# Optimization experiments

Measured on AMD Instinct MI355X. Metric: run time of the kernel, lower is better.

Reference implementation:

```python
import jax, jax.numpy as jnp
import numpy as np

N_NODES = 100000
N_EDGES = 1600000
IN_FEATS = 64
HIDDEN = 128


def setup_inputs() -> dict:
    key = jax.random.key(0)
    k1, k2, k3, k4 = jax.random.split(key, 4)
    X = jax.random.normal(k1, (N_NODES, IN_FEATS), dtype=jnp.float32)
    edge_index = jax.random.randint(k2, (2, N_EDGES), 0, N_NODES, dtype=jnp.int64)
    W1 = jax.random.normal(k3, (IN_FEATS, HIDDEN), dtype=jnp.float32) * (1.0 / np.sqrt(IN_FEATS))
    b1 = jnp.zeros((HIDDEN,), dtype=jnp.float32)
    W2 = jax.random.normal(k4, (HIDDEN, 1), dtype=jnp.float32) * (1.0 / np.sqrt(HIDDEN))
    b2 = jnp.zeros((1,), dtype=jnp.float32)
    return {"X": X, "edge_index": edge_index, "W1": W1, "b1": b1, "W2": W2, "b2": b2}


def _gcn_conv(X, src, dst, norm, W, b, n_nodes):
    # GCNConv: out = D^{-1/2} (A + I) D^{-1/2} (X @ W) + b
    h = X @ W                       # [N, out_feats]
    msg = h[src] * norm[:, None]    # gather + per-edge scale
    out = jax.ops.segment_sum(msg, dst, num_segments=n_nodes)
    return out + b


def _norm_and_loops(edge_index, n_nodes):
    # add self loops and compute symmetric normalization coefficients
    loop = jnp.arange(n_nodes, dtype=edge_index.dtype)
    src = jnp.concatenate([edge_index[0], loop])
    dst = jnp.concatenate([edge_index[1], loop])
    deg = jax.ops.segment_sum(jnp.ones_like(dst, dtype=jnp.float32), dst,
                              num_segments=n_nodes)  # deg >= 1 (self loop)
    dinv = jax.lax.rsqrt(deg)
    norm = dinv[src] * dinv[dst]    # [E + N]
    return src, dst, norm


def reference(X, edge_index, W1, b1, W2, b2):
    n_nodes = X.shape[0]
    src, dst, norm = _norm_and_loops(edge_index, n_nodes)
    h = jax.nn.relu(_gcn_conv(X, src, dst, norm, W1, b1, n_nodes))
    # dropout omitted (stochastic; identity for deterministic reference)
    out = _gcn_conv(h, src, dst, norm, W2, b2, n_nodes)
    return out
```

## Files before the change

kernel.cpp:

```cpp
#include <hip/hip_runtime.h>
#include <hip/hip_fp16.h>


#define NNODES 100000
#define INF 64
#define HID 128
#define MAXBK 128
#define TILE_E 16384

using half8 = __attribute__((ext_vector_type(8))) _Float16;
using f32x4 = __attribute__((ext_vector_type(4))) float;

__global__ __launch_bounds__(1024) void k_thist(const int* __restrict__ dstA,
                                                int* __restrict__ tileCnt, int nE) {
    __shared__ int h[MAXBK];
    int tid = threadIdx.x;
    if (tid < MAXBK) h[tid] = 0;
    __syncthreads();
    int base = blockIdx.x * TILE_E;
#pragma unroll
    for (int k = 0; k < 16; ++k) {
        int e = base + k * 1024 + tid;
        if (e < nE) atomicAdd(&h[((unsigned)dstA[e]) >> 10], 1);
    }
    __syncthreads();
    if (tid < MAXBK) tileCnt[blockIdx.x * MAXBK + tid] = h[tid];
}

__global__ __launch_bounds__(1024) void k_bscan(const int* __restrict__ tileCnt,
                                                int* __restrict__ tileBase,
                                                int* __restrict__ bBase,
                                                int* __restrict__ rowPtr,
                                                int n, int nbk, int nt) {
    __shared__ int part[8][MAXBK];
    __shared__ int colScan[MAXBK];
    int b = threadIdx.x & (MAXBK - 1);
    int tg = threadIdx.x >> 7;
    int cpg = (nt + 7) / 8;
    int tlo = tg * cpg, thi = min(tlo + cpg, nt);
    int sum = 0;
    for (int t = tlo; t < thi; ++t) sum += tileCnt[t * MAXBK + b];
    part[tg][b] = sum;
    __syncthreads();
    int coff = 0;
    for (int g = 0; g < tg; ++g) coff += part[g][b];
    int ctot = 0;
#pragma unroll
    for (int g = 0; g < 8; ++g) ctot += part[g][b];
    if (tg == 0) colScan[b] = ctot;
    __syncthreads();
    for (int off = 1; off < MAXBK; off <<= 1) {
        int u = (tg == 0 && b >= off) ? colScan[b - off] : 0;
        __syncthreads();
        if (tg == 0) colScan[b] += u;
        __syncthreads();
    }
    int colBase = colScan[b] - ctot;
    if (tg == 0 && b < nbk) bBase[b] = colBase;
    if (tg == 0 && b == nbk - 1) { bBase[nbk] = colScan[b]; rowPtr[n] = colScan[b]; }
    int run = colBase + coff;
    for (int t = tlo; t < thi; ++t) {
        tileBase[t * MAXBK + b] = run;
        run += tileCnt[t * MAXBK + b];
    }
}

__global__ __launch_bounds__(1024) void k_bin(const int* __restrict__ srcA,
                                              const int* __restrict__ dstA,
                                              const int* __restrict__ tileBase,
                                              unsigned* __restrict__ binned, int nE) {
    __shared__ int myb[MAXBK];
    __shared__ int cur[MAXBK];
    int tid = threadIdx.x;
    if (tid < MAXBK) {
        myb[tid] = tileBase[blockIdx.x * MAXBK + tid];
        cur[tid] = 0;
    }
    __syncthreads();
    int base = blockIdx.x * TILE_E;
#pragma unroll
    for (int k = 0; k < 16; ++k) {
        int e = base + k * 1024 + tid;
        if (e < nE) {
            int d = dstA[e];
            int s = srcA[e];
            int bk = ((unsigned)d) >> 10;
            int off = atomicAdd(&cur[bk], 1);
            binned[myb[bk] + off] = ((unsigned)(d & 1023) << 17) | (unsigned)s;
        }
    }
}

__global__ __launch_bounds__(1024) void k_csr(const unsigned* __restrict__ binned,
                                              const int* __restrict__ bBase,
                                              int* __restrict__ rowPtr,
                                              float* __restrict__ dinv,
                                              int* __restrict__ eSrc, int n) {
    __shared__ int hist[1024];
    __shared__ int curs[1024];
    int tid = threadIdx.x;
    int b = blockIdx.x;
    int lo = bBase[b], hi = bBase[b + 1];
    hist[tid] = 0;
    __syncthreads();
    for (int i = lo + tid; i < hi; i += 1024)
        atomicAdd(&hist[binned[i] >> 17], 1);
    __syncthreads();
    int own = hist[tid];
    for (int off = 1; off < 1024; off <<= 1) {
        int u = (tid >= off) ? hist[tid - off] : 0;
        __syncthreads();
        hist[tid] += u;
        __syncthreads();
    }
    int pos0 = lo + hist[tid] - own;
    curs[tid] = pos0;
    int node = (b << 10) + tid;
    if (node < n) {
        rowPtr[node] = pos0;
        dinv[node] = rsqrtf((float)(own + 1));
    }
    __syncthreads();
    for (int i = lo + tid; i < hi; i += 1024) {
        unsigned v = binned[i];
        int pos = atomicAdd(&curs[v >> 17], 1);
        eSrc[pos] = (int)(v & 0x1FFFFu);
    }
}

__global__ void k_prescale(const float4* __restrict__ X4, const float* __restrict__ dinv,
                           uint4* __restrict__ Xs4, const float* __restrict__ W1,
                           _Float16* __restrict__ W1t, int n) {
    int t = blockIdx.x * blockDim.x + threadIdx.x;
    if (t < n * 8) {
        int node = t >> 3;
        int r = t & 7;
        float dD = dinv[node];
        float4 a = X4[(size_t)node * 16 + r * 2];
        float4 b = X4[(size_t)node * 16 + r * 2 + 1];
        __half2 h0 = __float22half2_rn(make_float2(dD * a.x, dD * a.y));
        __half2 h1 = __float22half2_rn(make_float2(dD * a.z, dD * a.w));
        __half2 h2 = __float22half2_rn(make_float2(dD * b.x, dD * b.y));
        __half2 h3 = __float22half2_rn(make_float2(dD * b.z, dD * b.w));
        uint4 o;
        o.x = *(unsigned*)&h0; o.y = *(unsigned*)&h1;
        o.z = *(unsigned*)&h2; o.w = *(unsigned*)&h3;
        Xs4[t] = o;
    } else {
        int i = t - n * 8;
        if (i < HID * INF) {
            int nCol = i >> 6;
            int k = i & 63;
            W1t[i] = (_Float16)W1[k * HID + nCol];
        }
    }
}

__device__ inline void acc8_add(const uint4& v, float* acc) {
    const __half2* hp = (const __half2*)&v;
#pragma unroll
    for (int i = 0; i < 4; ++i) {
        float2 f = __half22float2(hp[i]);
        acc[2 * i]     += f.x;
        acc[2 * i + 1] += f.y;
    }
}

__global__ __launch_bounds__(256) void k_agg_mlp(const uint4* __restrict__ Xs4,
                                                 const int* __restrict__ rowPtr,
                                                 const int* __restrict__ eSrc,
                                                 const float* __restrict__ dinv,
                                                 const uint4* __restrict__ W1t4,
                                                 const float* __restrict__ b1,
                                                 const float* __restrict__ W2,
                                                 float* __restrict__ svs, int n) {
    __shared__ __align__(16) unsigned short W1s[HID * INF];
    __shared__ __align__(16) unsigned short aggS[32 * INF];
    __shared__ float b1s[HID];
    __shared__ float W2s[HID];
    int tid = threadIdx.x;

    for (int i = tid; i < HID * 8; i += 256) {
        int c = i >> 3, cb = i & 7;
        uint4 v = W1t4[i];
        int off = c * 128 + ((cb * 16) ^ ((c & 7) << 4));
        *(uint4*)((char*)W1s + off) = v;
    }
    if (tid < HID) {
        b1s[tid] = b1[tid];
        W2s[tid] = W2[tid];
    }

    int node0 = blockIdx.x * 32;
    int w = tid >> 3;
    int r = tid & 7;
    int node = node0 + w;
    if (node < n) {
        int beg = rowPtr[node];
        int end = rowPtr[node + 1];
        float dD = dinv[node];
        float acc[8];
        {
            uint4 v = Xs4[(size_t)node * 8 + r];
            const __half2* hp = (const __half2*)&v;
#pragma unroll
            for (int i = 0; i < 4; ++i) {
                float2 f = __half22float2(hp[i]);
                acc[2 * i] = f.x;
                acc[2 * i + 1] = f.y;
            }
        }
        int j = beg;
        int aEnd = min(end, (beg + 3) & ~3);
        for (; j < aEnd; ++j) {
            uint4 v = Xs4[(size_t)eSrc[j] * 8 + r];
            acc8_add(v, acc);
        }
        for (; j + 3 < end; j += 4) {
            int4 s4 = *(const int4*)(eSrc + j);
            uint4 v0 = Xs4[(size_t)s4.x * 8 + r];
            uint4 v1 = Xs4[(size_t)s4.y * 8 + r];
            uint4 v2 = Xs4[(size_t)s4.z * 8 + r];
            uint4 v3 = Xs4[(size_t)s4.w * 8 + r];
            acc8_add(v0, acc); acc8_add(v1, acc); acc8_add(v2, acc); acc8_add(v3, acc);
        }
        for (; j < end; ++j) {
            uint4 v = Xs4[(size_t)eSrc[j] * 8 + r];
            acc8_add(v, acc);
        }
        __half2 h0 = __float22half2_rn(make_float2(dD * acc[0], dD * acc[1]));
        __half2 h1 = __float22half2_rn(make_float2(dD * acc[2], dD * acc[3]));
        __half2 h2 = __float22half2_rn(make_float2(dD * acc[4], dD * acc[5]));
        __half2 h3 = __float22half2_rn(make_float2(dD * acc[6], dD * acc[7]));
        uint4 o;
        o.x = *(unsigned*)&h0; o.y = *(unsigned*)&h1;
        o.z = *(unsigned*)&h2; o.w = *(unsigned*)&h3;
        int off = w * 128 + ((r * 16) ^ ((w & 7) << 4));
        *(uint4*)((char*)aggS + off) = o;
    }
    __syncthreads();

    int wave = tid >> 6;
    if (wave < 2) {
        int l = tid & 63;
        int row16 = l & 15;
        int kg = l >> 4;
        int lrow = wave * 16 + row16;
        int swzA = (lrow & 7) << 4;
        half8 a0 = *(const half8*)((const char*)aggS + lrow * 128 + ((kg * 16) ^ swzA));
        half8 a1 = *(const half8*)((const char*)aggS + lrow * 128 + ((64 + kg * 16) ^ swzA));
        float p0 = 0.0f, p1 = 0.0f, p2 = 0.0f, p3 = 0.0f;
#pragma unroll
        for (int nt = 0; nt < 8; ++nt) {
            int c = nt * 16 + row16;
            int swzB = (c & 7) << 4;
            half8 bf0 = *(const half8*)((const char*)W1s + c * 128 + ((kg * 16) ^ swzB));
            half8 bf1 = *(const half8*)((const char*)W1s + c * 128 + ((64 + kg * 16) ^ swzB));
            f32x4 acc4 = {0.0f, 0.0f, 0.0f, 0.0f};
            acc4 = __builtin_amdgcn_mfma_f32_16x16x32_f16(a0, bf0, acc4, 0, 0, 0);
            acc4 = __builtin_amdgcn_mfma_f32_16x16x32_f16(a1, bf1, acc4, 0, 0, 0);
            float b1v = b1s[c];
            float w2v = W2s[c];
            float h;
            h = fmaxf(acc4[0] + b1v, 0.0f); p0 = fmaf(h, w2v, p0);
            h = fmaxf(acc4[1] + b1v, 0.0f); p1 = fmaf(h, w2v, p1);
            h = fmaxf(acc4[2] + b1v, 0.0f); p2 = fmaf(h, w2v, p2);
            h = fmaxf(acc4[3] + b1v, 0.0f); p3 = fmaf(h, w2v, p3);
        }
#pragma unroll
        for (int off = 1; off < 16; off <<= 1) {
            p0 += __shfl_xor(p0, off, 64);
            p1 += __shfl_xor(p1, off, 64);
            p2 += __shfl_xor(p2, off, 64);
            p3 += __shfl_xor(p3, off, 64);
        }
        if (row16 == 0) {
            int nd = node0 + wave * 16 + kg * 4;
            if (nd + 0 < n) svs[nd + 0] = dinv[nd + 0] * p0;
            if (nd + 1 < n) svs[nd + 1] = dinv[nd + 1] * p1;
            if (nd + 2 < n) svs[nd + 2] = dinv[nd + 2] * p2;
            if (nd + 3 < n) svs[nd + 3] = dinv[nd + 3] * p3;
        }
    }
}

__global__ __launch_bounds__(256) void k_out(const int* __restrict__ rowPtr,
                                             const int* __restrict__ eSrc,
                                             const float* __restrict__ dinv,
                                             const float* __restrict__ svs,
                                             const float* __restrict__ b2,
                                             float* __restrict__ out, int n) {
    int t = blockIdx.x * blockDim.x + threadIdx.x;
    int node = t >> 4;
    int r = t & 15;
    if (node >= n) return;
    int beg = rowPtr[node];
    int end = rowPtr[node + 1];
    float p = 0.0f;
    for (int j = beg + r; j < end; j += 16) p += svs[eSrc[j]];
    p += __shfl_xor(p, 1, 16);
    p += __shfl_xor(p, 2, 16);
    p += __shfl_xor(p, 4, 16);
    p += __shfl_xor(p, 8, 16);
    if (r == 0) {
        float dD = dinv[node];
        out[node] = fmaf(dD, p + svs[node], b2[0]);
    }
}

extern "C" void kernel_launch(void* const* d_in, const int* in_sizes, int n_in,
                              void* d_out, int out_size, void* d_ws, size_t ws_size,
                              hipStream_t stream) {
    const float* X  = (const float*)d_in[0];
    const int*   ei = (const int*)d_in[1];
    const float* W1 = (const float*)d_in[2];
    const float* b1 = (const float*)d_in[3];
    const float* W2 = (const float*)d_in[4];
    const float* b2 = (const float*)d_in[5];

    int N = in_sizes[0] / INF;
    int E = in_sizes[1] / 2;
    const int* srcA = ei;
    const int* dstA = ei + E;

    int nt  = (E + TILE_E - 1) / TILE_E;
    int nbk = (N + 1023) >> 10;

    uint4*    Xs4      = (uint4*)d_ws;
    unsigned* binned   = (unsigned*)(Xs4 + (size_t)N * 8);
    int*      eSrc     = (int*)(binned + E);
    _Float16* W1t      = (_Float16*)(eSrc + E);
    int*      tileCnt  = (int*)(W1t + HID * INF);
    int*      tileBase = tileCnt + nt * MAXBK;
    int*      bBase    = tileBase + nt * MAXBK;
    int*      rowPtr   = bBase + nbk + 1;
    float*    dinv     = (float*)(rowPtr + N + 1);
    float*    svs      = dinv + N;
    float*    out      = (float*)d_out;

    k_thist<<<nt, 1024, 0, stream>>>(dstA, tileCnt, E);
    k_bscan<<<1, 1024, 0, stream>>>(tileCnt, tileBase, bBase, rowPtr, N, nbk, nt);
    k_bin<<<nt, 1024, 0, stream>>>(srcA, dstA, tileBase, binned, E);
    k_csr<<<nbk, 1024, 0, stream>>>(binned, bBase, rowPtr, dinv, eSrc, N);
    k_prescale<<<(N * 8 + HID * INF + 255) / 256, 256, 0, stream>>>(
        (const float4*)X, dinv, Xs4, W1, W1t, N);
    k_agg_mlp<<<(N + 31) / 32, 256, 0, stream>>>(Xs4, rowPtr, eSrc, dinv,
                                                 (const uint4*)W1t, b1, W2, svs, N);
    k_out<<<(N * 16 + 255) / 256, 256, 0, stream>>>(rowPtr, eSrc, dinv, svs, b2, out, N);
}
```

Before: 112.6 us.

## Fuse CSR build and prescale into one cooperative kernel with grid syncs

Merges the five preprocessing kernels (tile histogram, bucket scan, binning, per-bucket CSR, prescale) into one cooperative kernel separated by grid.sync, keeping dst/src edge values in registers between the histogram and binning phases so they are not reloaded. This removes four kernel launches and their gaps, plus one pass over the edge arrays. The grid is only max(nt, nbk) ≈ 98 blocks of 1024 threads, so the prescale phase runs with far fewer threads than before, and the single-block scan phase leaves the other blocks idle. It also unrolls the aggregation gather loop to 8 edges per iteration to keep more loads in flight.

Measured after the change: 172.2 us. 1.53x slower.

```diff
diff --git a/kernel.cpp b/kernel.cpp
--- a/kernel.cpp
+++ b/kernel.cpp
@@ -1,5 +1,6 @@
 #include <hip/hip_runtime.h>
 #include <hip/hip_fp16.h>
+#include <hip/hip_cooperative_groups.h>
 
 
 #define NNODES 100000
@@ -8,147 +9,146 @@
 #define MAXBK 128
 #define TILE_E 16384
 
+namespace cg = cooperative_groups;
+
 using half8 = __attribute__((ext_vector_type(8))) _Float16;
 using f32x4 = __attribute__((ext_vector_type(4))) float;
 
-__global__ __launch_bounds__(1024) void k_thist(const int* __restrict__ dstA,
-                                                int* __restrict__ tileCnt, int nE) {
-    __shared__ int h[MAXBK];
+__global__ __launch_bounds__(1024, 1) void k_build(
+        const int* __restrict__ srcA, const int* __restrict__ dstA,
+        const float4* __restrict__ X4, const float* __restrict__ W1,
+        int* __restrict__ tileCnt, int* __restrict__ tileBase,
+        int* __restrict__ bBase, int* __restrict__ rowPtr,
+        float* __restrict__ dinv, unsigned* __restrict__ binned,
+        int* __restrict__ eSrc, uint4* __restrict__ Xs4,
+        _Float16* __restrict__ W1t, int n, int nE, int nt, int nbk) {
+    cg::grid_group grid = cg::this_grid();
+    __shared__ int lds[1024];
+    __shared__ int lds2[1024];
     int tid = threadIdx.x;
-    if (tid < MAXBK) h[tid] = 0;
-    __syncthreads();
-    int base = blockIdx.x * TILE_E;
-#pragma unroll
-    for (int k = 0; k < 16; ++k) {
-        int e = base + k * 1024 + tid;
-        if (e < nE) atomicAdd(&h[((unsigned)dstA[e]) >> 10], 1);
-    }
-    __syncthreads();
-    if (tid < MAXBK) tileCnt[blockIdx.x * MAXBK + tid] = h[tid];
-}
-
-__global__ __launch_bounds__(1024) void k_bscan(const int* __restrict__ tileCnt,
-                                                int* __restrict__ tileBase,
-                                                int* __restrict__ bBase,
-                                                int* __restrict__ rowPtr,
-                                                int n, int nbk, int nt) {
-    __shared__ int part[8][MAXBK];
-    __shared__ int colScan[MAXBK];
-    int b = threadIdx.x & (MAXBK - 1);
-    int tg = threadIdx.x >> 7;
-    int cpg = (nt + 7) / 8;
-    int tlo = tg * cpg, thi = min(tlo + cpg, nt);
-    int sum = 0;
-    for (int t = tlo; t < thi; ++t) sum += tileCnt[t * MAXBK + b];
-    part[tg][b] = sum;
-    __syncthreads();
-    int coff = 0;
-    for (int g = 0; g < tg; ++g) coff += part[g][b];
-    int ctot = 0;
-#pragma unroll
-    for (int g = 0; g < 8; ++g) ctot += part[g][b];
-    if (tg == 0) colScan[b] = ctot;
-    __syncthreads();
-    for (int off = 1; off < MAXBK; off <<= 1) {
-        int u = (tg == 0 && b >= off) ? colScan[b - off] : 0;
-        __syncthreads();
-        if (tg == 0) colScan[b] += u;
-        __syncthreads();
-    }
-    int colBase = colScan[b] - ctot;
-    if (tg == 0 && b < nbk) bBase[b] = colBase;
-    if (tg == 0 && b == nbk - 1) { bBase[nbk] = colScan[b]; rowPtr[n] = colScan[b]; }
-    int run = colBase + coff;
-    for (int t = tlo; t < thi; ++t) {
-        tileBase[t * MAXBK + b] = run;
-        run += tileCnt[t * MAXBK + b];
-    }
-}
-
-__global__ __launch_bounds__(1024) void k_bin(const int* __restrict__ srcA,
-                                              const int* __restrict__ dstA,
-                                              const int* __restrict__ tileBase,
-                                              unsigned* __restrict__ binned, int nE) {
-    __shared__ int myb[MAXBK];
-    __shared__ int cur[MAXBK];
-    int tid = threadIdx.x;
-    if (tid < MAXBK) {
-        myb[tid] = tileBase[blockIdx.x * MAXBK + tid];
-        cur[tid] = 0;
-    }
-    __syncthreads();
-    int base = blockIdx.x * TILE_E;
-#pragma unroll
-    for (int k = 0; k < 16; ++k) {
-        int e = base + k * 1024 + tid;
-        if (e < nE) {
-            int d = dstA[e];
-            int s = srcA[e];
-            int bk = ((unsigned)d) >> 10;
-            int off = atomicAdd(&cur[bk], 1);
-            binned[myb[bk] + off] = ((unsigned)(d & 1023) << 17) | (unsigned)s;
-        }
-    }
-}
-
-__global__ __launch_bounds__(1024) void k_csr(const unsigned* __restrict__ binned,
-                                              const int* __restrict__ bBase,
-                                              int* __restrict__ rowPtr,
-                                              float* __restrict__ dinv,
-                                              int* __restrict__ eSrc, int n) {
-    __shared__ int hist[1024];
-    __shared__ int curs[1024];
-    int tid = threadIdx.x;
-    int b = blockIdx.x;
-    int lo = bBase[b], hi = bBase[b + 1];
-    hist[tid] = 0;
-    __syncthreads();
-    for (int i = lo + tid; i < hi; i += 1024)
-        atomicAdd(&hist[binned[i] >> 17], 1);
-    __syncthreads();
-    int own = hist[tid];
-    for (int off = 1; off < 1024; off <<= 1) {
-        int u = (tid >= off) ? hist[tid - off] : 0;
-        __syncthreads();
-        hist[tid] += u;
-        __syncthreads();
-    }
-    int pos0 = lo + hist[tid] - own;
-    curs[tid] = pos0;
-    int node = (b << 10) + tid;
-    if (node < n) {
-        rowPtr[node] = pos0;
-        dinv[node] = rsqrtf((float)(own + 1));
-    }
-    __syncthreads();
-    for (int i = lo + tid; i < hi; i += 1024) {
-        unsigned v = binned[i];
-        int pos = atomicAdd(&curs[v >> 17], 1);
-        eSrc[pos] = (int)(v & 0x1FFFFu);
-    }
-}
-
-__global__ void k_prescale(const float4* __restrict__ X4, const float* __restrict__ dinv,
-                           uint4* __restrict__ Xs4, const float* __restrict__ W1,
-                           _Float16* __restrict__ W1t, int n) {
-    int t = blockIdx.x * blockDim.x + threadIdx.x;
-    if (t < n * 8) {
-        int node = t >> 3;
-        int r = t & 7;
-        float dD = dinv[node];
-        float4 a = X4[(size_t)node * 16 + r * 2];
-        float4 b = X4[(size_t)node * 16 + r * 2 + 1];
-        __half2 h0 = __float22half2_rn(make_float2(dD * a.x, dD * a.y));
-        __half2 h1 = __float22half2_rn(make_float2(dD * a.z, dD * a.w));
-        __half2 h2 = __float22half2_rn(make_float2(dD * b.x, dD * b.y));
-        __half2 h3 = __float22half2_rn(make_float2(dD * b.z, dD * b.w));
-        uint4 o;
-        o.x = *(unsigned*)&h0; o.y = *(unsigned*)&h1;
-        o.z = *(unsigned*)&h2; o.w = *(unsigned*)&h3;
-        Xs4[t] = o;
-    } else {
-        int i = t - n * 8;
-        if (i < HID * INF) {
+    int bx = blockIdx.x;
+
+    int dreg[16], sreg[16];
+    if (bx < nt) {
+        if (tid < MAXBK) lds[tid] = 0;
+        __syncthreads();
+        int base = bx * TILE_E;
+#pragma unroll
+        for (int k = 0; k < 16; ++k) {
+            int e = base + k * 1024 + tid;
+            if (e < nE) {
+                dreg[k] = dstA[e];
+                sreg[k] = srcA[e];
+                atomicAdd(&lds[((unsigned)dreg[k]) >> 10], 1);
+            } else {
+                dreg[k] = -1;
+            }
+        }
+        __syncthreads();
+        if (tid < MAXBK) tileCnt[bx * MAXBK + tid] = lds[tid];
+    }
+    grid.sync();
+
+    if (bx == 0) {
+        int b = tid & (MAXBK - 1);
+        int tg = tid >> 7;
+        int cpg = (nt + 7) / 8;
+        int tlo = tg * cpg, thi = min(tlo + cpg, nt);
+        int sum = 0;
+        for (int t = tlo; t < thi; ++t) sum += tileCnt[t * MAXBK + b];
+        lds[tg * MAXBK + b] = sum;
+        __syncthreads();
+        int coff = 0;
+        for (int g = 0; g < tg; ++g) coff += lds[g * MAXBK + b];
+        int ctot = 0;
+#pragma unroll
+        for (int g = 0; g < 8; ++g) ctot += lds[g * MAXBK + b];
+        if (tg == 0) lds2[b] = ctot;
+        __syncthreads();
+        for (int off = 1; off < MAXBK; off <<= 1) {
+            int u = (tg == 0 && b >= off) ? lds2[b - off] : 0;
+            __syncthreads();
+            if (tg == 0) lds2[b] += u;
+            __syncthreads();
+        }
+        int colBase = lds2[b] - ctot;
+        if (tg == 0 && b < nbk) bBase[b] = colBase;
+        if (tg == 0 && b == nbk - 1) { bBase[nbk] = lds2[b]; rowPtr[n] = lds2[b]; }
+        int run = colBase + coff;
+        for (int t = tlo; t < thi; ++t) {
+            tileBase[t * MAXBK + b] = run;
+            run += tileCnt[t * MAXBK + b];
+        }
+    }
+    grid.sync();
+
+    if (bx < nt) {
+        if (tid < MAXBK) {
+            lds[tid] = tileBase[bx * MAXBK + tid];
+            lds2[tid] = 0;
+        }
+        __syncthreads();
+#pragma unroll
+        for (int k = 0; k < 16; ++k) {
+            if (dreg[k] >= 0) {
+                int bk = ((unsigned)dreg[k]) >> 10;
+                int off = atomicAdd(&lds2[bk], 1);
+                binned[lds[bk] + off] =
+                    ((unsigned)(dreg[k] & 1023) << 17) | (unsigned)sreg[k];
+            }
+        }
+    }
+    grid.sync();
+
+    if (bx < nbk) {
+        int lo = bBase[bx], hi = bBase[bx + 1];
+        lds[tid] = 0;
+        __syncthreads();
+        for (int i = lo + tid; i < hi; i += 1024)
+            atomicAdd(&lds[binned[i] >> 17], 1);
+        __syncthreads();
+        int own = lds[tid];
+        for (int off = 1; off < 1024; off <<= 1) {
+            int u = (tid >= off) ? lds[tid - off] : 0;
+            __syncthreads();
+            lds[tid] += u;
+            __syncthreads();
+        }
+        int pos0 = lo + lds[tid] - own;
+        lds2[tid] = pos0;
+        int node = (bx << 10) + tid;
+        if (node < n) {
+            rowPtr[node] = pos0;
+            dinv[node] = rsqrtf((float)(own + 1));
+        }
+        __syncthreads();
+        for (int i = lo + tid; i < hi; i += 1024) {
+            unsigned v = binned[i];
+            int pos = atomicAdd(&lds2[v >> 17], 1);
+            eSrc[pos] = (int)(v & 0x1FFFFu);
+        }
+    }
+    grid.sync();
+
+    int stride = gridDim.x * 1024;
+    int totalE = n * 8 + HID * INF;
+    for (int t = bx * 1024 + tid; t < totalE; t += stride) {
+        if (t < n * 8) {
+            int node = t >> 3;
+            int r = t & 7;
+            float dD = dinv[node];
+            float4 a = X4[(size_t)node * 16 + r * 2];
+            float4 b = X4[(size_t)node * 16 + r * 2 + 1];
+            __half2 h0 = __float22half2_rn(make_float2(dD * a.x, dD * a.y));
+            __half2 h1 = __float22half2_rn(make_float2(dD * a.z, dD * a.w));
+            __half2 h2 = __float22half2_rn(make_float2(dD * b.x, dD * b.y));
+            __half2 h3 = __float22half2_rn(make_float2(dD * b.z, dD * b.w));
+            uint4 o;
+            o.x = *(unsigned*)&h0; o.y = *(unsigned*)&h1;
+            o.z = *(unsigned*)&h2; o.w = *(unsigned*)&h3;
+            Xs4[t] = o;
+        } else {
+            int i = t - n * 8;
             int nCol = i >> 6;
             int k = i & 63;
             W1t[i] = (_Float16)W1[k * HID + nCol];
@@ -216,13 +216,28 @@
             uint4 v = Xs4[(size_t)eSrc[j] * 8 + r];
             acc8_add(v, acc);
         }
-        for (; j + 3 < end; j += 4) {
+        for (; j + 7 < end; j += 8) {
+            int4 sa = *(const int4*)(eSrc + j);
+            int4 sb = *(const int4*)(eSrc + j + 4);
+            uint4 v0 = Xs4[(size_t)sa.x * 8 + r];
+            uint4 v1 = Xs4[(size_t)sa.y * 8 + r];
+            uint4 v2 = Xs4[(size_t)sa.z * 8 + r];
+            uint4 v3 = Xs4[(size_t)sa.w * 8 + r];
+            uint4 v4 = Xs4[(size_t)sb.x * 8 + r];
+            uint4 v5 = Xs4[(size_t)sb.y * 8 + r];
+            uint4 v6 = Xs4[(size_t)sb.z * 8 + r];
+            uint4 v7 = Xs4[(size_t)sb.w * 8 + r];
+            acc8_add(v0, acc); acc8_add(v1, acc); acc8_add(v2, acc); acc8_add(v3, acc);
+            acc8_add(v4, acc); acc8_add(v5, acc); acc8_add(v6, acc); acc8_add(v7, acc);
+        }
+        if (j + 3 < end) {
             int4 s4 = *(const int4*)(eSrc + j);
             uint4 v0 = Xs4[(size_t)s4.x * 8 + r];
             uint4 v1 = Xs4[(size_t)s4.y * 8 + r];
             uint4 v2 = Xs4[(size_t)s4.z * 8 + r];
             uint4 v3 = Xs4[(size_t)s4.w * 8 + r];
             acc8_add(v0, acc); acc8_add(v1, acc); acc8_add(v2, acc); acc8_add(v3, acc);
+            j += 4;
         }
         for (; j < end; ++j) {
             uint4 v = Xs4[(size_t)eSrc[j] * 8 + r];
@@ -338,12 +353,17 @@
     float*    svs      = dinv + N;
     float*    out      = (float*)d_out;
 
-    k_thist<<<nt, 1024, 0, stream>>>(dstA, tileCnt, E);
-    k_bscan<<<1, 1024, 0, stream>>>(tileCnt, tileBase, bBase, rowPtr, N, nbk, nt);
-    k_bin<<<nt, 1024, 0, stream>>>(srcA, dstA, tileBase, binned, E);
-    k_csr<<<nbk, 1024, 0, stream>>>(binned, bBase, rowPtr, dinv, eSrc, N);
-    k_prescale<<<(N * 8 + HID * INF + 255) / 256, 256, 0, stream>>>(
-        (const float4*)X, dinv, Xs4, W1, W1t, N);
+    int gridB = max(nt, nbk);
+    const float4* X4c = (const float4*)X;
+    void* args[] = {
+        (void*)&srcA, (void*)&dstA, (void*)&X4c, (void*)&W1,
+        (void*)&tileCnt, (void*)&tileBase, (void*)&bBase, (void*)&rowPtr,
+        (void*)&dinv, (void*)&binned, (void*)&eSrc, (void*)&Xs4,
+        (void*)&W1t, (void*)&N, (void*)&E, (void*)&nt, (void*)&nbk
+    };
+    hipLaunchCooperativeKernel((const void*)k_build, dim3(gridB), dim3(1024),
+                               args, 0, stream);
+
     k_agg_mlp<<<(N + 31) / 32, 256, 0, stream>>>(Xs4, rowPtr, eSrc, dinv,
                                                  (const uint4*)W1t, b1, W2, svs, N);
     k_out<<<(N * 16 + 255) / 256, 256, 0, stream>>>(rowPtr, eSrc, dinv, svs, b2, out, N);
```

## Fuse prescale into CSR build, fold W1 transpose into histogram, unroll gather by 8

Applied to the files above, without the earlier changes.

Removes the separate prescale kernel. The CSR kernel keeps each bucket's dinv values in shared memory and converts that bucket's 1024 node rows of X to half precision itself. The W1 transpose moves into an extra block of the histogram kernel. The aggregation gather loop is unrolled to 8 edges per iteration to put more loads in flight. This cuts one launch and a dinv reload, but puts the X conversion on only about 98 blocks, which may lower the bandwidth that part gets.

Result: no change. 113.1 us (+0.5%).

```diff
diff --git a/kernel.cpp b/kernel.cpp
--- a/kernel.cpp
+++ b/kernel.cpp
@@ -12,19 +12,30 @@
 using f32x4 = __attribute__((ext_vector_type(4))) float;
 
 __global__ __launch_bounds__(1024) void k_thist(const int* __restrict__ dstA,
-                                                int* __restrict__ tileCnt, int nE) {
+                                                int* __restrict__ tileCnt, int nE,
+                                                const float* __restrict__ W1,
+                                                _Float16* __restrict__ W1t, int nt) {
     __shared__ int h[MAXBK];
     int tid = threadIdx.x;
+    int bx = blockIdx.x;
+    if (bx == nt) {
+        for (int i = tid; i < HID * INF; i += 1024) {
+            int nCol = i >> 6;
+            int k = i & 63;
+            W1t[i] = (_Float16)W1[k * HID + nCol];
+        }
+        return;
+    }
     if (tid < MAXBK) h[tid] = 0;
     __syncthreads();
-    int base = blockIdx.x * TILE_E;
+    int base = bx * TILE_E;
 #pragma unroll
     for (int k = 0; k < 16; ++k) {
         int e = base + k * 1024 + tid;
         if (e < nE) atomicAdd(&h[((unsigned)dstA[e]) >> 10], 1);
     }
     __syncthreads();
-    if (tid < MAXBK) tileCnt[blockIdx.x * MAXBK + tid] = h[tid];
+    if (tid < MAXBK) tileCnt[bx * MAXBK + tid] = h[tid];
 }
 
 __global__ __launch_bounds__(1024) void k_bscan(const int* __restrict__ tileCnt,
@@ -95,7 +106,9 @@
                                               const int* __restrict__ bBase,
                                               int* __restrict__ rowPtr,
                                               float* __restrict__ dinv,
-                                              int* __restrict__ eSrc, int n) {
+                                              int* __restrict__ eSrc,
+                                              const float4* __restrict__ X4,
+                                              uint4* __restrict__ Xs4, int n) {
     __shared__ int hist[1024];
     __shared__ int curs[1024];
     int tid = threadIdx.x;
@@ -115,10 +128,12 @@
     }
     int pos0 = lo + hist[tid] - own;
     curs[tid] = pos0;
+    float dD = rsqrtf((float)(own + 1));
+    hist[tid] = (int)__float_as_uint(dD);
     int node = (b << 10) + tid;
     if (node < n) {
         rowPtr[node] = pos0;
-        dinv[node] = rsqrtf((float)(own + 1));
+        dinv[node] = dD;
     }
     __syncthreads();
     for (int i = lo + tid; i < hi; i += 1024) {
@@ -126,32 +141,26 @@
         int pos = atomicAdd(&curs[v >> 17], 1);
         eSrc[pos] = (int)(v & 0x1FFFFu);
     }
-}
-
-__global__ void k_prescale(const float4* __restrict__ X4, const float* __restrict__ dinv,
-                           uint4* __restrict__ Xs4, const float* __restrict__ W1,
-                           _Float16* __restrict__ W1t, int n) {
-    int t = blockIdx.x * blockDim.x + threadIdx.x;
-    if (t < n * 8) {
-        int node = t >> 3;
-        int r = t & 7;
-        float dD = dinv[node];
-        float4 a = X4[(size_t)node * 16 + r * 2];
-        float4 b = X4[(size_t)node * 16 + r * 2 + 1];
-        __half2 h0 = __float22half2_rn(make_float2(dD * a.x, dD * a.y));
-        __half2 h1 = __float22half2_rn(make_float2(dD * a.z, dD * a.w));
-        __half2 h2 = __float22half2_rn(make_float2(dD * b.x, dD * b.y));
-        __half2 h3 = __float22half2_rn(make_float2(dD * b.z, dD * b.w));
-        uint4 o;
-        o.x = *(unsigned*)&h0; o.y = *(unsigned*)&h1;
-        o.z = *(unsigned*)&h2; o.w = *(unsigned*)&h3;
-        Xs4[t] = o;
-    } else {
-        int i = t - n * 8;
-        if (i < HID * INF) {
-            int nCol = i >> 6;
-            int k = i & 63;
-            W1t[i] = (_Float16)W1[k * HID + nCol];
+    __syncthreads();
+    int nbase = b << 10;
+#pragma unroll
+    for (int k2 = 0; k2 < 8; ++k2) {
+        int t2 = k2 * 1024 + tid;
+        int nl = t2 >> 3;
+        int r2 = t2 & 7;
+        int node2 = nbase + nl;
+        if (node2 < n) {
+            float dD2 = __uint_as_float((unsigned)hist[nl]);
+            float4 a = X4[(size_t)node2 * 16 + r2 * 2];
+            float4 bb = X4[(size_t)node2 * 16 + r2 * 2 + 1];
+            __half2 h0 = __float22half2_rn(make_float2(dD2 * a.x, dD2 * a.y));
+            __half2 h1 = __float22half2_rn(make_float2(dD2 * a.z, dD2 * a.w));
+            __half2 h2 = __float22half2_rn(make_float2(dD2 * bb.x, dD2 * bb.y));
+            __half2 h3 = __float22half2_rn(make_float2(dD2 * bb.z, dD2 * bb.w));
+            uint4 o;
+            o.x = *(unsigned*)&h0; o.y = *(unsigned*)&h1;
+            o.z = *(unsigned*)&h2; o.w = *(unsigned*)&h3;
+            Xs4[(size_t)node2 * 8 + r2] = o;
         }
     }
 }
@@ -216,13 +225,28 @@
             uint4 v = Xs4[(size_t)eSrc[j] * 8 + r];
             acc8_add(v, acc);
         }
-        for (; j + 3 < end; j += 4) {
+        for (; j + 7 < end; j += 8) {
+            int4 sa = *(const int4*)(eSrc + j);
+            int4 sb = *(const int4*)(eSrc + j + 4);
+            uint4 v0 = Xs4[(size_t)sa.x * 8 + r];
+            uint4 v1 = Xs4[(size_t)sa.y * 8 + r];
+            uint4 v2 = Xs4[(size_t)sa.z * 8 + r];
+            uint4 v3 = Xs4[(size_t)sa.w * 8 + r];
+            uint4 v4 = Xs4[(size_t)sb.x * 8 + r];
+            uint4 v5 = Xs4[(size_t)sb.y * 8 + r];
+            uint4 v6 = Xs4[(size_t)sb.z * 8 + r];
+            uint4 v7 = Xs4[(size_t)sb.w * 8 + r];
+            acc8_add(v0, acc); acc8_add(v1, acc); acc8_add(v2, acc); acc8_add(v3, acc);
+            acc8_add(v4, acc); acc8_add(v5, acc); acc8_add(v6, acc); acc8_add(v7, acc);
+        }
+        if (j + 3 < end) {
             int4 s4 = *(const int4*)(eSrc + j);
             uint4 v0 = Xs4[(size_t)s4.x * 8 + r];
             uint4 v1 = Xs4[(size_t)s4.y * 8 + r];
             uint4 v2 = Xs4[(size_t)s4.z * 8 + r];
             uint4 v3 = Xs4[(size_t)s4.w * 8 + r];
             acc8_add(v0, acc); acc8_add(v1, acc); acc8_add(v2, acc); acc8_add(v3, acc);
+            j += 4;
         }
         for (; j < end; ++j) {
             uint4 v = Xs4[(size_t)eSrc[j] * 8 + r];
@@ -338,12 +362,11 @@
     float*    svs      = dinv + N;
     float*    out      = (float*)d_out;
 
-    k_thist<<<nt, 1024, 0, stream>>>(dstA, tileCnt, E);
+    k_thist<<<nt + 1, 1024, 0, stream>>>(dstA, tileCnt, E, W1, W1t, nt);
     k_bscan<<<1, 1024, 0, stream>>>(tileCnt, tileBase, bBase, rowPtr, N, nbk, nt);
     k_bin<<<nt, 1024, 0, stream>>>(srcA, dstA, tileBase, binned, E);
-    k_csr<<<nbk, 1024, 0, stream>>>(binned, bBase, rowPtr, dinv, eSrc, N);
-    k_prescale<<<(N * 8 + HID * INF + 255) / 256, 256, 0, stream>>>(
-        (const float4*)X, dinv, Xs4, W1, W1t, N);
+    k_csr<<<nbk, 1024, 0, stream>>>(binned, bBase, rowPtr, dinv, eSrc,
+                                    (const float4*)X, Xs4, N);
     k_agg_mlp<<<(N + 31) / 32, 256, 0, stream>>>(Xs4, rowPtr, eSrc, dinv,
                                                  (const uint4*)W1t, b1, W2, svs, N);
     k_out<<<(N * 16 + 255) / 256, 256, 0, stream>>>(rowPtr, eSrc, dinv, svs, b2, out, N);
```
